# Performance work log

Hardware: AMD Instinct MI355X
Metric: run time of the kernel (lower is better)

## Reference

```python
import jax, jax.numpy as jnp
import numpy as np

B, T = 16384, 64
VOCAB, EMB, HID = 1001, 16, 1024


def setup_inputs() -> dict:
    key = jax.random.key(0)
    k1, k2, k3, k4, k5, k6 = jax.random.split(key, 6)
    xis = jax.random.randint(k1, (B, T), 0, VOCAB, dtype=jnp.int32)
    emb = jax.random.normal(k2, (VOCAB, EMB), dtype=jnp.float32)
    lif_w = jax.random.normal(k3, (EMB, HID), dtype=jnp.float32) / np.sqrt(EMB)
    lif_b = jax.random.normal(k4, (HID,), dtype=jnp.float32) * 0.01
    fc_w = jax.random.normal(k5, (HID, 1), dtype=jnp.float32) / np.sqrt(HID)
    fc_b = jax.random.normal(k6, (1,), dtype=jnp.float32) * 0.01
    alpha = jnp.float32(0.3)   # LIF membrane decay (soma_params='all_share' scalar)
    beta = jnp.float32(0.0)    # LIF additive bias
    return {"xis": xis, "emb": emb, "lif_w": lif_w, "lif_b": lif_b,
            "fc_w": fc_w, "fc_b": fc_b, "alpha": alpha, "beta": beta}


def reference(xis, emb, lif_w, lif_b, fc_w, fc_b, alpha, beta):
    # Per-timestep: embedding lookup -> FcLif (linear + LIF membrane recurrence,
    # analog mode) -> dropout (eval: identity) -> fc. Only the last timestep's
    # fc output is returned by the original loop; only v carries across steps.
    x_emb = emb[xis]                     # [B, T, EMB]
    x_tbd = jnp.swapaxes(x_emb, 0, 1)    # [T, B, EMB] for scan over time

    def step(v, x_t):
        x1 = x_t @ lif_w + lif_b         # [B, HID] synaptic current
        v = alpha * v + x1 + beta        # membrane update (reset(x1) -> v0 = 0)
        return v, None

    v0 = jnp.zeros((B, HID), dtype=x_emb.dtype)
    vT, _ = jax.lax.scan(step, v0, x_tbd)
    o = jax.nn.relu(vT)                  # analog (cmode='analog') soma output
    out = (o @ fc_w + fc_b)[:, 0]        # [B]
    return out
```

## Files before the change

### kernel.cpp

```cpp
#include <hip/hip_runtime.h>
#include <hip/hip_bf16.h>


#define BB    16384
#define TT    64
#define EMBD  16
#define HIDD  1024
#define NVOC  1001
#define ROWS  64
#define NTHR  512
#define NBLK  (BB / ROWS)
#define EPAD  20
#define HTPW  8

typedef __attribute__((ext_vector_type(8))) short          frag_ab;
typedef __attribute__((ext_vector_type(4))) float          frag_cd;
typedef __attribute__((ext_vector_type(4))) unsigned short us4;

__device__ __forceinline__ float bf2f(unsigned short u) {
    union { unsigned int i; float f; } x; x.i = ((unsigned int)u) << 16; return x.f;
}
__device__ __forceinline__ unsigned short f2b(float f) {
    __hip_bfloat16 h = __float2bfloat16(f);
    return __builtin_bit_cast(unsigned short, h);
}

__global__ __launch_bounds__(NTHR)
void ftt_kernel(const int* __restrict__ xis, const float* __restrict__ emb,
                const float* __restrict__ lif_w, const float* __restrict__ lif_b,
                const float* __restrict__ fc_w, const float* __restrict__ fc_b,
                const float* __restrict__ alpha_p, const float* __restrict__ beta_p,
                float* __restrict__ out)
{
    __shared__ unsigned short embl[NVOC * EPAD];
    __shared__ unsigned short xwb[ROWS * EMBD];
    __shared__ float red[ROWS / 16][8][16];

    const int tid  = threadIdx.x;
    const int row0 = blockIdx.x * ROWS;
    const float alpha = alpha_p[0];
    const float beta  = beta_p[0];

    float S = 0.f, pk = 1.f, a32 = 0.f;
    #pragma unroll 1
    for (int k = 0; k < TT; ++k) { if (k == 32) a32 = pk; S += pk; pk *= alpha; }

    for (int v = tid; v < NVOC; v += NTHR) {
        const float4* ep = (const float4*)(emb + (size_t)v * EMBD);
        #pragma unroll
        for (int q = 0; q < 4; ++q) {
            const float4 e = ep[q];
            us4 u = { f2b(e.x), f2b(e.y), f2b(e.z), f2b(e.w) };
            *(us4*)&embl[v * EPAD + q * 4] = u;
        }
    }

    const int lane = tid & 63;
    const int wave = tid >> 6;
    const int nn   = lane & 15;
    const int kg   = lane >> 4;

    frag_ab bfrag[HTPW];
    float   biasr[HTPW], fcwr[HTPW];
    #pragma unroll
    for (int j = 0; j < HTPW; ++j) {
        const int h = wave * (HTPW * 16) + j * 16 + nn;
        biasr[j] = S * (lif_b[h] + beta);
        fcwr[j]  = fc_w[h];
        frag_ab b = {0, 0, 0, 0, 0, 0, 0, 0};
        if (kg < 2) {
            #pragma unroll
            for (int i = 0; i < 8; ++i) {
                const int k = kg * 8 + i;
                b[i] = (short)f2b(lif_w[k * HIDD + h]);
            }
        }
        bfrag[j] = b;
    }
    __syncthreads();

    {
        const int r   = tid >> 3;
        const int sub = tid & 7;
        const int q   = sub & 3;
        const int H   = sub >> 2;
        const int4* xp = (const int4*)(xis + (size_t)(row0 + r) * TT + H * 32);
        float px = 0.f, py = 0.f, pz = 0.f, pw = 0.f;
        float w = 1.f;
        #pragma unroll
        for (int c = 7; c >= 0; --c) {
            const int4 iv = xp[c];
            { const us4 e = *(const us4*)&embl[iv.w * EPAD + q * 4];
              px += w * bf2f(e.x); py += w * bf2f(e.y);
              pz += w * bf2f(e.z); pw += w * bf2f(e.w); w *= alpha; }
            { const us4 e = *(const us4*)&embl[iv.z * EPAD + q * 4];
              px += w * bf2f(e.x); py += w * bf2f(e.y);
              pz += w * bf2f(e.z); pw += w * bf2f(e.w); w *= alpha; }
            { const us4 e = *(const us4*)&embl[iv.y * EPAD + q * 4];
              px += w * bf2f(e.x); py += w * bf2f(e.y);
              pz += w * bf2f(e.z); pw += w * bf2f(e.w); w *= alpha; }
            { const us4 e = *(const us4*)&embl[iv.x * EPAD + q * 4];
              px += w * bf2f(e.x); py += w * bf2f(e.y);
              pz += w * bf2f(e.z); pw += w * bf2f(e.w); w *= alpha; }
        }
        const float sc = H ? 1.f : a32;
        px *= sc; py *= sc; pz *= sc; pw *= sc;
        px += __shfl_xor(px, 4); py += __shfl_xor(py, 4);
        pz += __shfl_xor(pz, 4); pw += __shfl_xor(pw, 4);
        if (H == 0) {
            us4 u = { f2b(px), f2b(py), f2b(pz), f2b(pw) };
            *(us4*)&xwb[r * EMBD + q * 4] = u;
        }
    }
    __syncthreads();

    #pragma unroll
    for (int rt = 0; rt < ROWS / 16; ++rt) {
        frag_ab a = {0, 0, 0, 0, 0, 0, 0, 0};
        if (kg < 2)
            a = *(const frag_ab*)&xwb[(rt * 16 + nn) * EMBD + kg * 8];
        frag_cd pacc = {0.f, 0.f, 0.f, 0.f};
        #pragma unroll
        for (int j = 0; j < HTPW; ++j) {
            frag_cd z = {0.f, 0.f, 0.f, 0.f};
            frag_cd c = __builtin_amdgcn_mfma_f32_16x16x32_bf16(a, bfrag[j], z, 0, 0, 0);
            #pragma unroll
            for (int x = 0; x < 4; ++x)
                pacc[x] += fmaxf(c[x] + biasr[j], 0.f) * fcwr[j];
        }
        #pragma unroll
        for (int m = 1; m <= 8; m <<= 1) {
            #pragma unroll
            for (int x = 0; x < 4; ++x) pacc[x] += __shfl_xor(pacc[x], m);
        }
        if (nn == 0) {
            #pragma unroll
            for (int x = 0; x < 4; ++x)
                red[rt][wave][kg * 4 + x] = pacc[x];
        }
    }
    __syncthreads();

    if (tid < ROWS) {
        float s = fc_b[0];
        #pragma unroll
        for (int w2 = 0; w2 < 8; ++w2) s += red[tid >> 4][w2][tid & 15];
        out[row0 + tid] = s;
    }
}

extern "C" void kernel_launch(void* const* d_in, const int* in_sizes, int n_in,
                              void* d_out, int out_size, void* d_ws, size_t ws_size,
                              hipStream_t stream) {
    const int*   xis   = (const int*)d_in[0];
    const float* emb   = (const float*)d_in[1];
    const float* lif_w = (const float*)d_in[2];
    const float* lif_b = (const float*)d_in[3];
    const float* fc_w  = (const float*)d_in[4];
    const float* fc_b  = (const float*)d_in[5];
    const float* alpha = (const float*)d_in[6];
    const float* beta  = (const float*)d_in[7];
    float* out = (float*)d_out;

    ftt_kernel<<<NBLK, NTHR, 0, stream>>>(
        xis, emb, lif_w, lif_b, fc_w, fc_b, alpha, beta, out);
}
```

Measured before the change: 15.21 us.

## Gather embeddings from global memory instead of staging the table in LDS

Drops the per-block copy of the full embedding table into shared memory as bf16; the weighted time sum now reads fp32 embedding rows straight from global/L2. Rows per block are halved to 32, doubling the block count, and the time sum is split across four chunks combined by shuffles. The geometric sum is computed in closed form, and the bias is folded into the MFMA accumulator initializer. Without the large LDS footprint more blocks can be resident at once, but the gathers now depend on cache hit rates. The weight fragments are also rebuilt by twice as many blocks.

```diff
diff --git a/kernel.cpp b/kernel.cpp
--- a/kernel.cpp
+++ b/kernel.cpp
@@ -6,59 +6,50 @@
 #define TT    64
 #define EMBD  16
 #define HIDD  1024
-#define NVOC  1001
-#define ROWS  64
+#define ROWS  32
 #define NTHR  512
 #define NBLK  (BB / ROWS)
-#define EPAD  20
+#define XWPAD 24
 #define HTPW  8
 
 typedef __attribute__((ext_vector_type(8))) short          frag_ab;
 typedef __attribute__((ext_vector_type(4))) float          frag_cd;
 typedef __attribute__((ext_vector_type(4))) unsigned short us4;
 
-__device__ __forceinline__ float bf2f(unsigned short u) {
-    union { unsigned int i; float f; } x; x.i = ((unsigned int)u) << 16; return x.f;
-}
 __device__ __forceinline__ unsigned short f2b(float f) {
     __hip_bfloat16 h = __float2bfloat16(f);
     return __builtin_bit_cast(unsigned short, h);
 }
 
-__global__ __launch_bounds__(NTHR)
+__global__ __launch_bounds__(NTHR, 4)
 void ftt_kernel(const int* __restrict__ xis, const float* __restrict__ emb,
                 const float* __restrict__ lif_w, const float* __restrict__ lif_b,
                 const float* __restrict__ fc_w, const float* __restrict__ fc_b,
                 const float* __restrict__ alpha_p, const float* __restrict__ beta_p,
                 float* __restrict__ out)
 {
-    __shared__ unsigned short embl[NVOC * EPAD];
-    __shared__ unsigned short xwb[ROWS * EMBD];
+    __shared__ unsigned short xwb[ROWS * XWPAD];
     __shared__ float red[ROWS / 16][8][16];
 
     const int tid  = threadIdx.x;
+    const int lane = tid & 63;
+    const int wave = tid >> 6;
     const int row0 = blockIdx.x * ROWS;
     const float alpha = alpha_p[0];
     const float beta  = beta_p[0];
 
-    float S = 0.f, pk = 1.f, a32 = 0.f;
-    #pragma unroll 1
-    for (int k = 0; k < TT; ++k) { if (k == 32) a32 = pk; S += pk; pk *= alpha; }
+    const float a2  = alpha * alpha;
+    const float a4  = a2 * a2;
+    const float a8  = a4 * a4;
+    const float a16 = a8 * a8;
+    const float a32 = a16 * a16;
+    const float a48 = a32 * a16;
+    const float a64 = a32 * a32;
+    const float S   = (fabsf(1.f - alpha) < 1e-8f) ? (float)TT
+                                                   : (1.f - a64) / (1.f - alpha);
 
-    for (int v = tid; v < NVOC; v += NTHR) {
-        const float4* ep = (const float4*)(emb + (size_t)v * EMBD);
-        #pragma unroll
-        for (int q = 0; q < 4; ++q) {
-            const float4 e = ep[q];
-            us4 u = { f2b(e.x), f2b(e.y), f2b(e.z), f2b(e.w) };
-            *(us4*)&embl[v * EPAD + q * 4] = u;
-        }
-    }
-
-    const int lane = tid & 63;
-    const int wave = tid >> 6;
-    const int nn   = lane & 15;
-    const int kg   = lane >> 4;
+    const int nn = lane & 15;
+    const int kg = lane >> 4;
 
     frag_ab bfrag[HTPW];
     float   biasr[HTPW], fcwr[HTPW];
@@ -70,46 +61,42 @@
         frag_ab b = {0, 0, 0, 0, 0, 0, 0, 0};
         if (kg < 2) {
             #pragma unroll
-            for (int i = 0; i < 8; ++i) {
-                const int k = kg * 8 + i;
-                b[i] = (short)f2b(lif_w[k * HIDD + h]);
-            }
+            for (int i = 0; i < 8; ++i)
+                b[i] = (short)f2b(lif_w[(kg * 8 + i) * HIDD + h]);
         }
         bfrag[j] = b;
     }
-    __syncthreads();
 
     {
-        const int r   = tid >> 3;
-        const int sub = tid & 7;
+        const int r   = tid >> 4;
+        const int sub = tid & 15;
+        const int c   = sub >> 2;
         const int q   = sub & 3;
-        const int H   = sub >> 2;
-        const int4* xp = (const int4*)(xis + (size_t)(row0 + r) * TT + H * 32);
-        float px = 0.f, py = 0.f, pz = 0.f, pw = 0.f;
+        const int4* xp = (const int4*)(xis + (size_t)(row0 + r) * TT + c * 16);
+        const float* eb = emb + q * 4;
+        float ax = 0.f, ay = 0.f, az = 0.f, aw = 0.f;
         float w = 1.f;
         #pragma unroll
-        for (int c = 7; c >= 0; --c) {
-            const int4 iv = xp[c];
-            { const us4 e = *(const us4*)&embl[iv.w * EPAD + q * 4];
-              px += w * bf2f(e.x); py += w * bf2f(e.y);
-              pz += w * bf2f(e.z); pw += w * bf2f(e.w); w *= alpha; }
-            { const us4 e = *(const us4*)&embl[iv.z * EPAD + q * 4];
-              px += w * bf2f(e.x); py += w * bf2f(e.y);
-              pz += w * bf2f(e.z); pw += w * bf2f(e.w); w *= alpha; }
-            { const us4 e = *(const us4*)&embl[iv.y * EPAD + q * 4];
-              px += w * bf2f(e.x); py += w * bf2f(e.y);
-              pz += w * bf2f(e.z); pw += w * bf2f(e.w); w *= alpha; }
-            { const us4 e = *(const us4*)&embl[iv.x * EPAD + q * 4];
-              px += w * bf2f(e.x); py += w * bf2f(e.y);
-              pz += w * bf2f(e.z); pw += w * bf2f(e.w); w *= alpha; }
+        for (int cc = 3; cc >= 0; --cc) {
+            const int4 iv = xp[cc];
+            { const float4 e = *(const float4*)(eb + ((size_t)iv.w << 4));
+              ax += w * e.x; ay += w * e.y; az += w * e.z; aw += w * e.w; w *= alpha; }
+            { const float4 e = *(const float4*)(eb + ((size_t)iv.z << 4));
+              ax += w * e.x; ay += w * e.y; az += w * e.z; aw += w * e.w; w *= alpha; }
+            { const float4 e = *(const float4*)(eb + ((size_t)iv.y << 4));
+              ax += w * e.x; ay += w * e.y; az += w * e.z; aw += w * e.w; w *= alpha; }
+            { const float4 e = *(const float4*)(eb + ((size_t)iv.x << 4));
+              ax += w * e.x; ay += w * e.y; az += w * e.z; aw += w * e.w; w *= alpha; }
         }
-        const float sc = H ? 1.f : a32;
-        px *= sc; py *= sc; pz *= sc; pw *= sc;
-        px += __shfl_xor(px, 4); py += __shfl_xor(py, 4);
-        pz += __shfl_xor(pz, 4); pw += __shfl_xor(pw, 4);
-        if (H == 0) {
-            us4 u = { f2b(px), f2b(py), f2b(pz), f2b(pw) };
-            *(us4*)&xwb[r * EMBD + q * 4] = u;
+        const float sc = (c == 3) ? 1.f : ((c == 2) ? a16 : ((c == 1) ? a32 : a48));
+        ax *= sc; ay *= sc; az *= sc; aw *= sc;
+        ax += __shfl_xor(ax, 4); ay += __shfl_xor(ay, 4);
+        az += __shfl_xor(az, 4); aw += __shfl_xor(aw, 4);
+        ax += __shfl_xor(ax, 8); ay += __shfl_xor(ay, 8);
+        az += __shfl_xor(az, 8); aw += __shfl_xor(aw, 8);
+        if (c == 0) {
+            us4 u = { f2b(ax), f2b(ay), f2b(az), f2b(aw) };
+            *(us4*)&xwb[r * XWPAD + q * 4] = u;
         }
     }
     __syncthreads();
@@ -118,15 +105,15 @@
     for (int rt = 0; rt < ROWS / 16; ++rt) {
         frag_ab a = {0, 0, 0, 0, 0, 0, 0, 0};
         if (kg < 2)
-            a = *(const frag_ab*)&xwb[(rt * 16 + nn) * EMBD + kg * 8];
+            a = *(const frag_ab*)&xwb[(rt * 16 + nn) * XWPAD + kg * 8];
         frag_cd pacc = {0.f, 0.f, 0.f, 0.f};
         #pragma unroll
         for (int j = 0; j < HTPW; ++j) {
-            frag_cd z = {0.f, 0.f, 0.f, 0.f};
+            frag_cd z = { biasr[j], biasr[j], biasr[j], biasr[j] };
             frag_cd c = __builtin_amdgcn_mfma_f32_16x16x32_bf16(a, bfrag[j], z, 0, 0, 0);
             #pragma unroll
             for (int x = 0; x < 4; ++x)
-                pacc[x] += fmaxf(c[x] + biasr[j], 0.f) * fcwr[j];
+                pacc[x] += fmaxf(c[x], 0.f) * fcwr[j];
         }
         #pragma unroll
         for (int m = 1; m <= 8; m <<= 1) {
```

After: 16.18 us. +6.4%, slower.
